# Performance work log

Measured on AMD Instinct MI355X. Metric: run time of the kernel, lower is better.

The kernel has to match this reference:

```python
import jax, jax.numpy as jnp
import numpy as np

N = 50000
E = 800000
IN_C = 128
HID = 8
HEADS = 8
OUT_C = 16
NEG_SLOPE = 0.2


def setup_inputs() -> dict:
    key = jax.random.key(0)
    ks = jax.random.split(key, 10)
    x = jax.random.normal(ks[0], (N, IN_C), dtype=jnp.float32)
    edge_index = jax.random.randint(ks[1], (2, E), 0, N, dtype=jnp.int64)
    # layer 1: GATConv(IN_C, HID, heads=HEADS, concat=True)
    s1 = 1.0 / np.sqrt(IN_C)
    W1 = jax.random.normal(ks[2], (HEADS * HID, IN_C), dtype=jnp.float32) * s1
    att_src1 = jax.random.normal(ks[3], (HEADS, HID), dtype=jnp.float32) * 0.1
    att_dst1 = jax.random.normal(ks[4], (HEADS, HID), dtype=jnp.float32) * 0.1
    b1 = jnp.zeros((HEADS * HID,), dtype=jnp.float32)
    # layer 2: GATConv(HEADS*HID, OUT_C, heads=1, concat=False)
    s2 = 1.0 / np.sqrt(HEADS * HID)
    W2 = jax.random.normal(ks[5], (OUT_C, HEADS * HID), dtype=jnp.float32) * s2
    att_src2 = jax.random.normal(ks[6], (1, OUT_C), dtype=jnp.float32) * 0.1
    att_dst2 = jax.random.normal(ks[7], (1, OUT_C), dtype=jnp.float32) * 0.1
    b2 = jnp.zeros((OUT_C,), dtype=jnp.float32)
    return {"x": x, "edge_index": edge_index, "W1": W1, "att_src1": att_src1,
            "att_dst1": att_dst1, "b1": b1, "W2": W2, "att_src2": att_src2,
            "att_dst2": att_dst2, "b2": b2}


def _gat_conv(x, W, att_src, att_dst, bias, src, dst, concat):
    # x: [N, F_in]; W: [H*C, F_in]; att_*: [H, C]
    H, C = att_src.shape
    h = (x @ W.T).reshape(N, H, C)                       # [N, H, C]
    a_src = jnp.einsum('nhc,hc->nh', h, att_src)          # [N, H]
    a_dst = jnp.einsum('nhc,hc->nh', h, att_dst)          # [N, H]
    e = a_src[src] + a_dst[dst]                           # [Etot, H]
    e = jnp.where(e > 0, e, NEG_SLOPE * e)                # LeakyReLU(0.2)
    # segment softmax over edges grouped by destination node
    m = jax.ops.segment_max(e, dst, num_segments=N)       # [N, H]
    e = jnp.exp(e - m[dst])
    denom = jax.ops.segment_sum(e, dst, num_segments=N)   # [N, H]
    alpha = e / (denom[dst] + 1e-16)                      # [Etot, H]
    msg = alpha[:, :, None] * h[src]                      # [Etot, H, C]
    out = jax.ops.segment_sum(msg, dst, num_segments=N)   # [N, H, C]
    if concat:
        out = out.reshape(N, H * C)
    else:
        out = out.mean(axis=1)
    return out + bias


def reference(x, edge_index, W1, att_src1, att_dst1, b1, W2, att_src2, att_dst2, b2):
    # add self-loops (PyG GATConv default)
    loops = jnp.arange(N, dtype=edge_index.dtype)
    src = jnp.concatenate([edge_index[0], loops])
    dst = jnp.concatenate([edge_index[1], loops])
    h = _gat_conv(x, W1, att_src1, att_dst1, b1, src, dst, concat=True)
    h = jax.nn.elu(h)  # dropout is identity in eval mode
    return _gat_conv(h, W2, att_src2, att_dst2, b2, src, dst, concat=False)
```

## Files before the change

kernel.cpp:

```cpp
#include <hip/hip_runtime.h>
#include <hip/hip_fp16.h>
#include <math.h>

#define NN 50000
#define NE 800000
#define ETOT (NE + NN)
#define INC 128
#define F1 64
#define NH 8
#define OC 16
#define NEG 0.2f
#define BSH 7
#define NBUK 391
#define CHUNK_A 4096
#define NBLK_A ((ETOT + CHUNK_A - 1) / CHUNK_A)
#define G1TILE 64
#define NBLK_G1 ((NN + G1TILE - 1) / G1TILE)
#define XR 136

typedef _Float16 half8 __attribute__((ext_vector_type(8)));
typedef float f32x4 __attribute__((ext_vector_type(4)));

__device__ __forceinline__ float leaky(float x){ return x > 0.f ? x : NEG * x; }

__device__ __forceinline__ void getsd(const int* __restrict__ ei, int e, int& s, int& d){
    if (e < NE){ s = ei[e]; d = ei[NE + e]; }
    else { s = e - NE; d = s; }
}


__global__ __launch_bounds__(256) void zero_gbcnt(int* __restrict__ gbcnt){
    int i = blockIdx.x*256 + threadIdx.x;
    if (i < NBUK) gbcnt[i] = 0;
}

__global__ __launch_bounds__(256) void bucket_hist(const int* __restrict__ ei, int* __restrict__ gbcnt){
    __shared__ int bcnt[NBUK];
    int tid = threadIdx.x;
    for (int j = tid; j < NBUK; j += 256) bcnt[j] = 0;
    __syncthreads();
    int e0 = blockIdx.x * CHUNK_A;
    int e1 = e0 + CHUNK_A; if (e1 > ETOT) e1 = ETOT;
    for (int e = e0 + tid; e < e1; e += 256){
        int d = (e < NE) ? ei[NE + e] : e - NE;
        atomicAdd(&bcnt[d >> BSH], 1);
    }
    __syncthreads();
    for (int j = tid; j < NBUK; j += 256)
        if (bcnt[j]) atomicAdd(&gbcnt[j], bcnt[j]);
}

__global__ __launch_bounds__(512) void bucket_scan(const int* __restrict__ gbcnt,
        int* __restrict__ gboff, int* __restrict__ gbcur){
    __shared__ int s[512];
    int t = threadIdx.x;
    int v = (t < NBUK) ? gbcnt[t] : 0;
    s[t] = v; __syncthreads();
    for (int off = 1; off < 512; off <<= 1){
        int u = (t >= off) ? s[t - off] : 0;
        __syncthreads();
        s[t] += u;
        __syncthreads();
    }
    if (t < NBUK){ int ex = s[t] - v; gboff[t] = ex; gbcur[t] = ex; }
    if (t == 0) gboff[NBUK] = ETOT;
}

__global__ __launch_bounds__(256) void scatter_gemm1(const int* __restrict__ ei,
        int* __restrict__ gbcur, unsigned* __restrict__ packed,
        const float* __restrict__ x, const float* __restrict__ W1,
        const float* __restrict__ att_s, const float* __restrict__ att_d,
        __half* __restrict__ h1h, float* __restrict__ a_src, float* __restrict__ a_dst){
    __shared__ _Float16 xs[64*XR];
    __shared__ _Float16 wsl[64*XR];
    int tid = threadIdx.x;
    if (blockIdx.x < NBLK_A){
        int* bcnt = (int*)xs;
        for (int j = tid; j < NBUK; j += 256) bcnt[j] = 0;
        __syncthreads();
        int e0 = blockIdx.x * CHUNK_A;
        int e1 = e0 + CHUNK_A; if (e1 > ETOT) e1 = ETOT;
        for (int e = e0 + tid; e < e1; e += 256){
            int d = (e < NE) ? ei[NE + e] : e - NE;
            atomicAdd(&bcnt[d >> BSH], 1);
        }
        __syncthreads();
        for (int j = tid; j < NBUK; j += 256){
            int c = bcnt[j];
            bcnt[j] = c ? atomicAdd(&gbcur[j], c) : 0;
        }
        __syncthreads();
        for (int e = e0 + tid; e < e1; e += 256){
            int s, d; getsd(ei, e, s, d);
            int pos = atomicAdd(&bcnt[d >> BSH], 1);
            packed[pos] = ((unsigned)s << 16) | (unsigned)d;
        }
        return;
    }
    int base = (blockIdx.x - NBLK_A) * G1TILE;
    for (int i = tid; i < F1*INC; i += 256){
        int o = i >> 7, k = i & 127;
        wsl[o*XR + k] = (_Float16)W1[i];
    }
    for (int f = tid; f < 64*32; f += 256){
        int row = f >> 5, c4 = f & 31;
        int n = base + row;
        float4 v = (n < NN) ? reinterpret_cast<const float4*>(x)[n*32 + c4]
                            : make_float4(0.f,0.f,0.f,0.f);
        _Float16* p = &xs[row*XR + c4*4];
        p[0] = (_Float16)v.x; p[1] = (_Float16)v.y;
        p[2] = (_Float16)v.z; p[3] = (_Float16)v.w;
    }
    __syncthreads();
    int w = tid >> 6, lane = tid & 63;
    int mrow = lane & 15, kg = lane >> 4;
    int nodeb = w*16;
    half8 afrag[4];
    #pragma unroll
    for (int kk = 0; kk < 4; ++kk){
        const _Float16* pa = &xs[(nodeb + mrow)*XR + kk*32 + kg*4];
        *(unsigned long long*)&afrag[kk]       = *(const unsigned long long*)pa;
        *((unsigned long long*)&afrag[kk] + 1) = *(const unsigned long long*)(pa + 16);
    }
    f32x4 acc[4];
    #pragma unroll
    for (int ot = 0; ot < 4; ++ot) acc[ot] = (f32x4){0.f,0.f,0.f,0.f};
    #pragma unroll
    for (int ot = 0; ot < 4; ++ot){
        #pragma unroll
        for (int kk = 0; kk < 4; ++kk){
            const _Float16* pb = &wsl[(ot*16 + mrow)*XR + kk*32 + kg*4];
            half8 bfrag;
            *(unsigned long long*)&bfrag       = *(const unsigned long long*)pb;
            *((unsigned long long*)&bfrag + 1) = *(const unsigned long long*)(pb + 16);
            acc[ot] = __builtin_amdgcn_mfma_f32_16x16x32_f16(afrag[kk], bfrag, acc[ot], 0, 0, 0);
        }
    }
    #pragma unroll
    for (int ot = 0; ot < 4; ++ot){
        int o = ot*16 + mrow;
        float as_o = att_s[o], ad_o = att_d[o];
        #pragma unroll
        for (int r = 0; r < 4; ++r){
            float dv = acc[ot][r];
            int node = base + nodeb + kg*4 + r;
            if (node < NN) h1h[node*64 + o] = __float2half(dv);
            float ps = dv * as_o, pd = dv * ad_o;
            ps += __shfl_xor(ps, 1); ps += __shfl_xor(ps, 2); ps += __shfl_xor(ps, 4);
            pd += __shfl_xor(pd, 1); pd += __shfl_xor(pd, 2); pd += __shfl_xor(pd, 4);
            if ((lane & 7) == 0 && node < NN){
                int h = ot*2 + ((lane >> 3) & 1);
                a_src[node*8 + h] = ps;
                a_dst[node*8 + h] = pd;
            }
        }
    }
}

__global__ __launch_bounds__(256) void bucket_finalize(const unsigned* __restrict__ packed,
        const int* __restrict__ gboff, int* __restrict__ rowstart, int* __restrict__ esrc){
    __shared__ int ldeg[1 << BSH];
    __shared__ int lcur[1 << BSH];
    __shared__ int wtot[2];
    int b = blockIdx.x, t = threadIdx.x;
    if (t < (1 << BSH)) ldeg[t] = 0;
    __syncthreads();
    int p0 = gboff[b], p1 = gboff[b+1];
    for (int i = p0 + t; i < p1; i += 256)
        atomicAdd(&ldeg[packed[i] & ((1 << BSH) - 1)], 1);
    __syncthreads();
    if (t < (1 << BSH)){
        int v = ldeg[t];
        int lane = t & 63, w = t >> 6;
        int iv = v;
        #pragma unroll
        for (int off = 1; off < 64; off <<= 1){
            int u = __shfl_up(iv, off);
            if (lane >= off) iv += u;
        }
        lcur[t] = iv;
        if (lane == 63) wtot[w] = iv;
    }
    __syncthreads();
    if (t < (1 << BSH)){
        int v = ldeg[t];
        int w = t >> 6;
        int incl = lcur[t] + (w ? wtot[0] : 0);
        int rs = p0 + incl - v;
        int n = (b << BSH) + t;
        if (n < NN) rowstart[n] = rs;
        lcur[t] = rs;
    }
    if (b == 0 && t == 0) rowstart[NN] = ETOT;
    __syncthreads();
    for (int i = p0 + t; i < p1; i += 256){
        unsigned p = packed[i];
        int pos = atomicAdd(&lcur[p & ((1 << BSH) - 1)], 1);
        esrc[pos] = (int)(p >> 16);
    }
}


__global__ __launch_bounds__(256, 4) void gemm2(const float* __restrict__ out1, const float* __restrict__ W2,
        const float* __restrict__ att_s, const float* __restrict__ att_d,
        __half* __restrict__ h2h, float* __restrict__ a_src, float* __restrict__ a_dst){
    __shared__ float xs2[64*80];
    int tid = threadIdx.x;
    int base = blockIdx.x * 64;
    int w = tid >> 6, lane = tid & 63;
    int o = lane >> 2, ks = lane & 3;
    float4 wr[4];
    {
        const float4* W4 = reinterpret_cast<const float4*>(W2);
        #pragma unroll
        for (int j4 = 0; j4 < 4; ++j4)
            wr[j4] = W4[o*16 + ks*4 + j4];
    }
    float as_o = att_s[o], ad_o = att_d[o];
    {
        #pragma unroll
        for (int j = 0; j < 4; ++j){
            int f = tid + 256*j;
            int row = f >> 4, c4 = f & 15;
            int n = base + row;
            float4 v = make_float4(0.f,0.f,0.f,0.f);
            if (n < NN) v = reinterpret_cast<const float4*>(out1)[n*16 + c4];
            v.x = v.x > 0.f ? v.x : __expf(v.x) - 1.f;
            v.y = v.y > 0.f ? v.y : __expf(v.y) - 1.f;
            v.z = v.z > 0.f ? v.z : __expf(v.z) - 1.f;
            v.w = v.w > 0.f ? v.w : __expf(v.w) - 1.f;
            int sk = c4 >> 2, j4 = c4 & 3;
            *(float4*)(&xs2[row*80 + sk*20 + j4*4]) = v;
        }
    }
    __syncthreads();
    for (int r = 0; r < 16; ++r){
        int row = w*16 + r;
        const float* xb = &xs2[row*80 + ks*20];
        float acc = 0.f;
        #pragma unroll
        for (int j4 = 0; j4 < 4; ++j4){
            float4 xv = *(const float4*)(xb + j4*4);
            acc = fmaf(xv.x, wr[j4].x, acc);
            acc = fmaf(xv.y, wr[j4].y, acc);
            acc = fmaf(xv.z, wr[j4].z, acc);
            acc = fmaf(xv.w, wr[j4].w, acc);
        }
        acc += __shfl_xor(acc, 1); acc += __shfl_xor(acc, 2);
        int node = base + row;
        float ps = acc * as_o, pd = acc * ad_o;
        ps += __shfl_xor(ps, 4); ps += __shfl_xor(ps, 8);
        ps += __shfl_xor(ps, 16); ps += __shfl_xor(ps, 32);
        pd += __shfl_xor(pd, 4); pd += __shfl_xor(pd, 8);
        pd += __shfl_xor(pd, 16); pd += __shfl_xor(pd, 32);
        if (node < NN){
            if (ks == 0) h2h[node*16 + o] = __float2half(acc);
            if (lane == 0){ a_src[node] = ps; a_dst[node] = pd; }
        }
    }
}


__global__ __launch_bounds__(256) void layer1_node(const int* __restrict__ rowstart,
        const int* __restrict__ esrc, const float* __restrict__ a_src,
        const float* __restrict__ a_dst, const __half* __restrict__ h1h,
        const float* __restrict__ b1, float* __restrict__ out1){
    int wid = __builtin_amdgcn_readfirstlane((blockIdx.x*256 + threadIdx.x) >> 6);
    int lane = threadIdx.x & 63;
    if (wid >= NN) return;
    int n = wid;
    int h = lane >> 3;
    int r0 = rowstart[n], r1 = rowstart[n+1];
    float ad = a_dst[n*8 + h];
    float den0 = 0.f, acc0 = 0.f, den1 = 0.f, acc1 = 0.f;
    float den2 = 0.f, acc2 = 0.f, den3 = 0.f, acc3 = 0.f;
    float den4 = 0.f, acc4 = 0.f, den5 = 0.f, acc5 = 0.f;
    float den6 = 0.f, acc6 = 0.f, den7 = 0.f, acc7 = 0.f;
    int i = r0;
    int nfull = (r1 - r0) >> 3;
    if (nfull > 0){
        int s0 = esrc[i],   s1 = esrc[i+1], s2 = esrc[i+2], s3 = esrc[i+3];
        int s4 = esrc[i+4], s5 = esrc[i+5], s6 = esrc[i+6], s7 = esrc[i+7];
        float eA0 = a_src[s0*8 + h], eA1 = a_src[s1*8 + h];
        float eA2 = a_src[s2*8 + h], eA3 = a_src[s3*8 + h];
        float eA4 = a_src[s4*8 + h], eA5 = a_src[s5*8 + h];
        float eA6 = a_src[s6*8 + h], eA7 = a_src[s7*8 + h];
        float hA0 = __half2float(h1h[s0*64 + lane]);
        float hA1 = __half2float(h1h[s1*64 + lane]);
        float hA2 = __half2float(h1h[s2*64 + lane]);
        float hA3 = __half2float(h1h[s3*64 + lane]);
        float hA4 = __half2float(h1h[s4*64 + lane]);
        float hA5 = __half2float(h1h[s5*64 + lane]);
        float hA6 = __half2float(h1h[s6*64 + lane]);
        float hA7 = __half2float(h1h[s7*64 + lane]);
        i += 8;
        for (int b = 1; b < nfull; ++b){
            int t0 = esrc[i],   t1 = esrc[i+1], t2 = esrc[i+2], t3 = esrc[i+3];
            int t4 = esrc[i+4], t5 = esrc[i+5], t6 = esrc[i+6], t7 = esrc[i+7];
            float eB0 = a_src[t0*8 + h], eB1 = a_src[t1*8 + h];
            float eB2 = a_src[t2*8 + h], eB3 = a_src[t3*8 + h];
            float eB4 = a_src[t4*8 + h], eB5 = a_src[t5*8 + h];
            float eB6 = a_src[t6*8 + h], eB7 = a_src[t7*8 + h];
            float hB0 = __half2float(h1h[t0*64 + lane]);
            float hB1 = __half2float(h1h[t1*64 + lane]);
            float hB2 = __half2float(h1h[t2*64 + lane]);
            float hB3 = __half2float(h1h[t3*64 + lane]);
            float hB4 = __half2float(h1h[t4*64 + lane]);
            float hB5 = __half2float(h1h[t5*64 + lane]);
            float hB6 = __half2float(h1h[t6*64 + lane]);
            float hB7 = __half2float(h1h[t7*64 + lane]);
            i += 8;
            float p0 = __expf(leaky(eA0 + ad)), p1 = __expf(leaky(eA1 + ad));
            float p2 = __expf(leaky(eA2 + ad)), p3 = __expf(leaky(eA3 + ad));
            float p4 = __expf(leaky(eA4 + ad)), p5 = __expf(leaky(eA5 + ad));
            float p6 = __expf(leaky(eA6 + ad)), p7 = __expf(leaky(eA7 + ad));
            den0 += p0; acc0 = fmaf(p0, hA0, acc0);
            den1 += p1; acc1 = fmaf(p1, hA1, acc1);
            den2 += p2; acc2 = fmaf(p2, hA2, acc2);
            den3 += p3; acc3 = fmaf(p3, hA3, acc3);
            den4 += p4; acc4 = fmaf(p4, hA4, acc4);
            den5 += p5; acc5 = fmaf(p5, hA5, acc5);
            den6 += p6; acc6 = fmaf(p6, hA6, acc6);
            den7 += p7; acc7 = fmaf(p7, hA7, acc7);
            eA0 = eB0; eA1 = eB1; eA2 = eB2; eA3 = eB3;
            eA4 = eB4; eA5 = eB5; eA6 = eB6; eA7 = eB7;
            hA0 = hB0; hA1 = hB1; hA2 = hB2; hA3 = hB3;
            hA4 = hB4; hA5 = hB5; hA6 = hB6; hA7 = hB7;
        }
        float p0 = __expf(leaky(eA0 + ad)), p1 = __expf(leaky(eA1 + ad));
        float p2 = __expf(leaky(eA2 + ad)), p3 = __expf(leaky(eA3 + ad));
        float p4 = __expf(leaky(eA4 + ad)), p5 = __expf(leaky(eA5 + ad));
        float p6 = __expf(leaky(eA6 + ad)), p7 = __expf(leaky(eA7 + ad));
        den0 += p0; acc0 = fmaf(p0, hA0, acc0);
        den1 += p1; acc1 = fmaf(p1, hA1, acc1);
        den2 += p2; acc2 = fmaf(p2, hA2, acc2);
        den3 += p3; acc3 = fmaf(p3, hA3, acc3);
        den4 += p4; acc4 = fmaf(p4, hA4, acc4);
        den5 += p5; acc5 = fmaf(p5, hA5, acc5);
        den6 += p6; acc6 = fmaf(p6, hA6, acc6);
        den7 += p7; acc7 = fmaf(p7, hA7, acc7);
    }
    for (; i + 3 < r1; i += 4){
        int s0 = esrc[i], s1 = esrc[i+1], s2 = esrc[i+2], s3 = esrc[i+3];
        float e0 = leaky(a_src[s0*8 + h] + ad);
        float e1 = leaky(a_src[s1*8 + h] + ad);
        float e2 = leaky(a_src[s2*8 + h] + ad);
        float e3 = leaky(a_src[s3*8 + h] + ad);
        float hv0 = __half2float(h1h[s0*64 + lane]);
        float hv1 = __half2float(h1h[s1*64 + lane]);
        float hv2 = __half2float(h1h[s2*64 + lane]);
        float hv3 = __half2float(h1h[s3*64 + lane]);
        float p0 = __expf(e0), p1 = __expf(e1), p2 = __expf(e2), p3 = __expf(e3);
        den0 += p0; acc0 = fmaf(p0, hv0, acc0);
        den1 += p1; acc1 = fmaf(p1, hv1, acc1);
        den2 += p2; acc2 = fmaf(p2, hv2, acc2);
        den3 += p3; acc3 = fmaf(p3, hv3, acc3);
    }
    for (; i < r1; ++i){
        int s = esrc[i];
        float p = __expf(leaky(a_src[s*8 + h] + ad));
        den0 += p; acc0 = fmaf(p, __half2float(h1h[s*64 + lane]), acc0);
    }
    float den = ((den0 + den1) + (den2 + den3)) + ((den4 + den5) + (den6 + den7));
    float acc = ((acc0 + acc1) + (acc2 + acc3)) + ((acc4 + acc5) + (acc6 + acc7));
    out1[n*64 + lane] = acc/(den + 1e-16f) + b1[lane];
}

__global__ __launch_bounds__(256) void layer2_node(const int* __restrict__ rowstart,
        const int* __restrict__ esrc, const float* __restrict__ a_src,
        const float* __restrict__ a_dst, const __half* __restrict__ h2h,
        const float* __restrict__ b2, float* __restrict__ out){
    int wid = __builtin_amdgcn_readfirstlane((blockIdx.x*256 + threadIdx.x) >> 6);
    int lane = threadIdx.x & 63;
    if (wid >= NN) return;
    int n = wid;
    int slot = lane >> 4, c = lane & 15;
    int r0 = rowstart[n], r1 = rowstart[n+1];
    float ad = a_dst[n];
    float den0 = 0.f, acc0 = 0.f, den1 = 0.f, acc1 = 0.f;
    float den2 = 0.f, acc2 = 0.f, den3 = 0.f, acc3 = 0.f;
    int i = r0 + slot;
    if (i + 12 < r1){
        int s0 = esrc[i], s1 = esrc[i+4], s2 = esrc[i+8], s3 = esrc[i+12];
        float eA0 = a_src[s0], eA1 = a_src[s1], eA2 = a_src[s2], eA3 = a_src[s3];
        float hA0 = __half2float(h2h[s0*16 + c]);
        float hA1 = __half2float(h2h[s1*16 + c]);
        float hA2 = __half2float(h2h[s2*16 + c]);
        float hA3 = __half2float(h2h[s3*16 + c]);
        i += 16;
        while (i + 12 < r1){
            int t0 = esrc[i], t1 = esrc[i+4], t2 = esrc[i+8], t3 = esrc[i+12];
            float eB0 = a_src[t0], eB1 = a_src[t1], eB2 = a_src[t2], eB3 = a_src[t3];
            float hB0 = __half2float(h2h[t0*16 + c]);
            float hB1 = __half2float(h2h[t1*16 + c]);
            float hB2 = __half2float(h2h[t2*16 + c]);
            float hB3 = __half2float(h2h[t3*16 + c]);
            i += 16;
            float p0 = __expf(leaky(eA0 + ad)), p1 = __expf(leaky(eA1 + ad));
            float p2 = __expf(leaky(eA2 + ad)), p3 = __expf(leaky(eA3 + ad));
            den0 += p0; acc0 = fmaf(p0, hA0, acc0);
            den1 += p1; acc1 = fmaf(p1, hA1, acc1);
            den2 += p2; acc2 = fmaf(p2, hA2, acc2);
            den3 += p3; acc3 = fmaf(p3, hA3, acc3);
            eA0 = eB0; eA1 = eB1; eA2 = eB2; eA3 = eB3;
            hA0 = hB0; hA1 = hB1; hA2 = hB2; hA3 = hB3;
        }
        float p0 = __expf(leaky(eA0 + ad)), p1 = __expf(leaky(eA1 + ad));
        float p2 = __expf(leaky(eA2 + ad)), p3 = __expf(leaky(eA3 + ad));
        den0 += p0; acc0 = fmaf(p0, hA0, acc0);
        den1 += p1; acc1 = fmaf(p1, hA1, acc1);
        den2 += p2; acc2 = fmaf(p2, hA2, acc2);
        den3 += p3; acc3 = fmaf(p3, hA3, acc3);
    }
    for (; i < r1; i += 4){
        int s = esrc[i];
        float p = __expf(leaky(a_src[s] + ad));
        den0 += p; acc0 = fmaf(p, __half2float(h2h[s*16 + c]), acc0);
    }
    float den = (den0 + den1) + (den2 + den3);
    float acc = (acc0 + acc1) + (acc2 + acc3);
    den += __shfl_xor(den, 16); den += __shfl_xor(den, 32);
    acc += __shfl_xor(acc, 16); acc += __shfl_xor(acc, 32);
    if (slot == 0) out[n*16 + c] = acc/(den + 1e-16f) + b2[c];
}

extern "C" void kernel_launch(void* const* d_in, const int* in_sizes, int n_in,
                              void* d_out, int out_size, void* d_ws, size_t ws_size,
                              hipStream_t stream){
    const float* x    = (const float*)d_in[0];
    const int*   ei   = (const int*)d_in[1];
    const float* W1   = (const float*)d_in[2];
    const float* as1w = (const float*)d_in[3];
    const float* ad1w = (const float*)d_in[4];
    const float* b1   = (const float*)d_in[5];
    const float* W2   = (const float*)d_in[6];
    const float* as2w = (const float*)d_in[7];
    const float* ad2w = (const float*)d_in[8];
    const float* b2   = (const float*)d_in[9];
    float* out = (float*)d_out;

    float* ws = (float*)d_ws;
    __half* h1h     = (__half*)ws;
    float* out1     = ws + (size_t)32*NN;
    int*   rowstart = (int*)(ws + (size_t)96*NN);
    int*   gbcnt    = rowstart + NN + 1;
    int*   gboff    = gbcnt + NBUK;
    int*   gbcur    = gboff + NBUK + 1;
    unsigned* packed= (unsigned*)(gbcur + NBUK);
    int*   esrc     = (int*)(packed + ETOT);
    float* a_src1 = out;
    float* a_dst1 = out + (size_t)8*NN;
    __half* h2h   = h1h;
    float* a_src2 = ws + (size_t)8*NN;
    float* a_dst2 = a_src2 + NN;

    hipLaunchKernelGGL(zero_gbcnt,      dim3(2), dim3(256), 0, stream, gbcnt);
    hipLaunchKernelGGL(bucket_hist,     dim3(NBLK_A), dim3(256), 0, stream, ei, gbcnt);
    hipLaunchKernelGGL(bucket_scan,     dim3(1), dim3(512), 0, stream, gbcnt, gboff, gbcur);
    hipLaunchKernelGGL(scatter_gemm1,   dim3(NBLK_A + NBLK_G1), dim3(256), 0, stream,
                       ei, gbcur, packed, x, W1, as1w, ad1w, h1h, a_src1, a_dst1);
    hipLaunchKernelGGL(bucket_finalize, dim3(NBUK), dim3(256), 0, stream, packed, gboff, rowstart, esrc);

    hipLaunchKernelGGL(layer1_node, dim3((NN*64 + 255)/256), dim3(256), 0, stream,
                       rowstart, esrc, a_src1, a_dst1, h1h, b1, out1);
    hipLaunchKernelGGL(gemm2, dim3((NN + 63)/64), dim3(256), 0, stream, out1, W2, as2w, ad2w, h2h, a_src2, a_dst2);
    hipLaunchKernelGGL(layer2_node, dim3((NN*64 + 255)/256), dim3(256), 0, stream,
                       rowstart, esrc, a_src2, a_dst2, h2h, b2, out);
}
```

Before: 113.8 us.

## Split layer1 aggregation across two edge halves with half2 feature loads

The layer-1 aggregation kernel now has each half-wavefront process alternate edges, with every lane loading a half2 (two channels) rather than one half. The two partial sums are combined with a cross-half shuffle and written as float2. This halves the per-edge instruction count and doubles the bytes per gather load, and it drops the 8-deep software-pipelined unroll in favour of a simpler 4-edge loop, which may reduce memory-level parallelism per wave.

```diff
diff --git a/kernel.cpp b/kernel.cpp
--- a/kernel.cpp
+++ b/kernel.cpp
@@ -269,101 +269,68 @@
     int lane = threadIdx.x & 63;
     if (wid >= NN) return;
     int n = wid;
-    int h = lane >> 3;
+    int c2 = lane & 31;
+    int eh = lane >> 5;
+    int h = c2 >> 2;
     int r0 = rowstart[n], r1 = rowstart[n+1];
     float ad = a_dst[n*8 + h];
-    float den0 = 0.f, acc0 = 0.f, den1 = 0.f, acc1 = 0.f;
-    float den2 = 0.f, acc2 = 0.f, den3 = 0.f, acc3 = 0.f;
-    float den4 = 0.f, acc4 = 0.f, den5 = 0.f, acc5 = 0.f;
-    float den6 = 0.f, acc6 = 0.f, den7 = 0.f, acc7 = 0.f;
+    const __half2* h1h2 = (const __half2*)h1h;
+    float den0 = 0.f, x00 = 0.f, x01 = 0.f;
+    float den1 = 0.f, x10 = 0.f, x11 = 0.f;
+    float den2 = 0.f, x20 = 0.f, x21 = 0.f;
+    float den3 = 0.f, x30 = 0.f, x31 = 0.f;
     int i = r0;
-    int nfull = (r1 - r0) >> 3;
-    if (nfull > 0){
-        int s0 = esrc[i],   s1 = esrc[i+1], s2 = esrc[i+2], s3 = esrc[i+3];
-        int s4 = esrc[i+4], s5 = esrc[i+5], s6 = esrc[i+6], s7 = esrc[i+7];
-        float eA0 = a_src[s0*8 + h], eA1 = a_src[s1*8 + h];
-        float eA2 = a_src[s2*8 + h], eA3 = a_src[s3*8 + h];
-        float eA4 = a_src[s4*8 + h], eA5 = a_src[s5*8 + h];
-        float eA6 = a_src[s6*8 + h], eA7 = a_src[s7*8 + h];
-        float hA0 = __half2float(h1h[s0*64 + lane]);
-        float hA1 = __half2float(h1h[s1*64 + lane]);
-        float hA2 = __half2float(h1h[s2*64 + lane]);
-        float hA3 = __half2float(h1h[s3*64 + lane]);
-        float hA4 = __half2float(h1h[s4*64 + lane]);
-        float hA5 = __half2float(h1h[s5*64 + lane]);
-        float hA6 = __half2float(h1h[s6*64 + lane]);
-        float hA7 = __half2float(h1h[s7*64 + lane]);
-        i += 8;
-        for (int b = 1; b < nfull; ++b){
-            int t0 = esrc[i],   t1 = esrc[i+1], t2 = esrc[i+2], t3 = esrc[i+3];
-            int t4 = esrc[i+4], t5 = esrc[i+5], t6 = esrc[i+6], t7 = esrc[i+7];
-            float eB0 = a_src[t0*8 + h], eB1 = a_src[t1*8 + h];
-            float eB2 = a_src[t2*8 + h], eB3 = a_src[t3*8 + h];
-            float eB4 = a_src[t4*8 + h], eB5 = a_src[t5*8 + h];
-            float eB6 = a_src[t6*8 + h], eB7 = a_src[t7*8 + h];
-            float hB0 = __half2float(h1h[t0*64 + lane]);
-            float hB1 = __half2float(h1h[t1*64 + lane]);
-            float hB2 = __half2float(h1h[t2*64 + lane]);
-            float hB3 = __half2float(h1h[t3*64 + lane]);
-            float hB4 = __half2float(h1h[t4*64 + lane]);
-            float hB5 = __half2float(h1h[t5*64 + lane]);
-            float hB6 = __half2float(h1h[t6*64 + lane]);
-            float hB7 = __half2float(h1h[t7*64 + lane]);
-            i += 8;
-            float p0 = __expf(leaky(eA0 + ad)), p1 = __expf(leaky(eA1 + ad));
-            float p2 = __expf(leaky(eA2 + ad)), p3 = __expf(leaky(eA3 + ad));
-            float p4 = __expf(leaky(eA4 + ad)), p5 = __expf(leaky(eA5 + ad));
-            float p6 = __expf(leaky(eA6 + ad)), p7 = __expf(leaky(eA7 + ad));
-            den0 += p0; acc0 = fmaf(p0, hA0, acc0);
-            den1 += p1; acc1 = fmaf(p1, hA1, acc1);
-            den2 += p2; acc2 = fmaf(p2, hA2, acc2);
-            den3 += p3; acc3 = fmaf(p3, hA3, acc3);
-            den4 += p4; acc4 = fmaf(p4, hA4, acc4);
-            den5 += p5; acc5 = fmaf(p5, hA5, acc5);
-            den6 += p6; acc6 = fmaf(p6, hA6, acc6);
-            den7 += p7; acc7 = fmaf(p7, hA7, acc7);
-            eA0 = eB0; eA1 = eB1; eA2 = eB2; eA3 = eB3;
-            eA4 = eB4; eA5 = eB5; eA6 = eB6; eA7 = eB7;
-            hA0 = hB0; hA1 = hB1; hA2 = hB2; hA3 = hB3;
-            hA4 = hB4; hA5 = hB5; hA6 = hB6; hA7 = hB7;
-        }
-        float p0 = __expf(leaky(eA0 + ad)), p1 = __expf(leaky(eA1 + ad));
-        float p2 = __expf(leaky(eA2 + ad)), p3 = __expf(leaky(eA3 + ad));
-        float p4 = __expf(leaky(eA4 + ad)), p5 = __expf(leaky(eA5 + ad));
-        float p6 = __expf(leaky(eA6 + ad)), p7 = __expf(leaky(eA7 + ad));
-        den0 += p0; acc0 = fmaf(p0, hA0, acc0);
-        den1 += p1; acc1 = fmaf(p1, hA1, acc1);
-        den2 += p2; acc2 = fmaf(p2, hA2, acc2);
-        den3 += p3; acc3 = fmaf(p3, hA3, acc3);
-        den4 += p4; acc4 = fmaf(p4, hA4, acc4);
-        den5 += p5; acc5 = fmaf(p5, hA5, acc5);
-        den6 += p6; acc6 = fmaf(p6, hA6, acc6);
-        den7 += p7; acc7 = fmaf(p7, hA7, acc7);
-    }
-    for (; i + 3 < r1; i += 4){
-        int s0 = esrc[i], s1 = esrc[i+1], s2 = esrc[i+2], s3 = esrc[i+3];
-        float e0 = leaky(a_src[s0*8 + h] + ad);
-        float e1 = leaky(a_src[s1*8 + h] + ad);
-        float e2 = leaky(a_src[s2*8 + h] + ad);
-        float e3 = leaky(a_src[s3*8 + h] + ad);
-        float hv0 = __half2float(h1h[s0*64 + lane]);
-        float hv1 = __half2float(h1h[s1*64 + lane]);
-        float hv2 = __half2float(h1h[s2*64 + lane]);
-        float hv3 = __half2float(h1h[s3*64 + lane]);
-        float p0 = __expf(e0), p1 = __expf(e1), p2 = __expf(e2), p3 = __expf(e3);
-        den0 += p0; acc0 = fmaf(p0, hv0, acc0);
-        den1 += p1; acc1 = fmaf(p1, hv1, acc1);
-        den2 += p2; acc2 = fmaf(p2, hv2, acc2);
-        den3 += p3; acc3 = fmaf(p3, hv3, acc3);
-    }
-    for (; i < r1; ++i){
+    for (; i + 7 < r1; i += 8){
+        int s0 = esrc[i     + eh];
+        int s1 = esrc[i + 2 + eh];
+        int s2 = esrc[i + 4 + eh];
+        int s3 = esrc[i + 6 + eh];
+        float e0 = a_src[s0*8 + h];
+        float e1 = a_src[s1*8 + h];
+        float e2 = a_src[s2*8 + h];
+        float e3 = a_src[s3*8 + h];
+        float2 h0 = __half22float2(h1h2[s0*32 + c2]);
+        float2 h1 = __half22float2(h1h2[s1*32 + c2]);
+        float2 h2 = __half22float2(h1h2[s2*32 + c2]);
+        float2 h3 = __half22float2(h1h2[s3*32 + c2]);
+        float p0 = __expf(leaky(e0 + ad));
+        float p1 = __expf(leaky(e1 + ad));
+        float p2 = __expf(leaky(e2 + ad));
+        float p3 = __expf(leaky(e3 + ad));
+        den0 += p0; x00 = fmaf(p0, h0.x, x00); x01 = fmaf(p0, h0.y, x01);
+        den1 += p1; x10 = fmaf(p1, h1.x, x10); x11 = fmaf(p1, h1.y, x11);
+        den2 += p2; x20 = fmaf(p2, h2.x, x20); x21 = fmaf(p2, h2.y, x21);
+        den3 += p3; x30 = fmaf(p3, h3.x, x30); x31 = fmaf(p3, h3.y, x31);
+    }
+    for (; i + 1 < r1; i += 2){
+        int s = esrc[i + eh];
+        float e = a_src[s*8 + h];
+        float2 hv = __half22float2(h1h2[s*32 + c2]);
+        float p = __expf(leaky(e + ad));
+        den0 += p; x00 = fmaf(p, hv.x, x00); x01 = fmaf(p, hv.y, x01);
+    }
+    if (i < r1){
         int s = esrc[i];
-        float p = __expf(leaky(a_src[s*8 + h] + ad));
-        den0 += p; acc0 = fmaf(p, __half2float(h1h[s*64 + lane]), acc0);
-    }
-    float den = ((den0 + den1) + (den2 + den3)) + ((den4 + den5) + (den6 + den7));
-    float acc = ((acc0 + acc1) + (acc2 + acc3)) + ((acc4 + acc5) + (acc6 + acc7));
-    out1[n*64 + lane] = acc/(den + 1e-16f) + b1[lane];
+        float e = a_src[s*8 + h];
+        float2 hv = __half22float2(h1h2[s*32 + c2]);
+        float p = __expf(leaky(e + ad));
+        p = (eh == 0) ? p : 0.f;
+        den0 += p; x00 = fmaf(p, hv.x, x00); x01 = fmaf(p, hv.y, x01);
+    }
+    float den = (den0 + den1) + (den2 + den3);
+    float a0 = (x00 + x10) + (x20 + x30);
+    float a1 = (x01 + x11) + (x21 + x31);
+    den += __shfl_xor(den, 32);
+    a0  += __shfl_xor(a0, 32);
+    a1  += __shfl_xor(a1, 32);
+    if (eh == 0){
+        float2 bb = reinterpret_cast<const float2*>(b1)[c2];
+        float inv = 1.f/(den + 1e-16f);
+        float2 o;
+        o.x = a0*inv + bb.x;
+        o.y = a1*inv + bb.y;
+        reinterpret_cast<float2*>(out1)[n*32 + c2] = o;
+    }
 }
 
 __global__ __launch_bounds__(256) void layer2_node(const int* __restrict__ rowstart,
```

Result: no change. 115.2 us (+1.2%).
